# Performance work log

Hardware: AMD Instinct MI355X
Metric: run time of the kernel (lower is better)

Reference implementation:

```python
import jax, jax.numpy as jnp
import numpy as np

EPS = 1e-6
CLIP_RATIO = 1.0  # input_clip_ratio


def fwht(x):
    """Fast Walsh-Hadamard transform along last dim (N must be a power of 2).
    Unnormalized; caller divides by sqrt(N) (QuaRot OnlineHadamard convention)."""
    m, n = x.shape
    h = 1
    y = x
    while h < n:  # log2(n) fixed iterations, fine under jit
        y = y.reshape(m, n // (2 * h), 2, h)
        a, b = y[:, :, 0, :], y[:, :, 1, :]
        y = jnp.concatenate([a + b, a - b], axis=-1)  # [m, n//(2h), 2h]
        h *= 2
    return y.reshape(m, n)


def setup_inputs() -> dict:
    key = jax.random.key(0)
    k1, k2, k3 = jax.random.split(key, 3)
    M, IN, OUT = 8192, 4096, 4096
    x = jax.random.normal(k1, (M, IN), dtype=jnp.float32)
    weight = jax.random.normal(k2, (OUT, IN), dtype=jnp.float32) * 0.02
    bias = jax.random.normal(k3, (OUT,), dtype=jnp.float32) * 0.01
    return {"x": x, "weight": weight, "bias": bias}


def reference(x, weight, bias):
    # --- offline weight quantization (quantize_from_float) ---
    # per-output-row symmetric int4: scale = max|w| / 7, clamp min 1e-6
    w_scales = jnp.clip(jnp.max(jnp.abs(weight), axis=1, keepdims=True), EPS, None) / 7.0  # [OUT,1]
    qw = jnp.clip(jnp.round(weight / w_scales), -8, 7)  # int4 values kept in fp32 (exact)

    # --- online Hadamard rotation of activations ---
    n = x.shape[-1]
    x2 = fwht(x) * (1.0 / jnp.sqrt(jnp.float32(n)))

    # --- symmetric per-token int4 activation quantization (QuaRot Quantizer) ---
    sx = jnp.clip(jnp.max(jnp.abs(x2), axis=-1, keepdims=True), EPS, None) * (CLIP_RATIO / 7.0)  # [M,1]
    qx = jnp.clip(jnp.round(x2 / sx), -8, 7)

    qy = jnp.einsum('mk,nk->mn', qx, qw)  # [M, OUT]

    # --- sym_dequant: row scale (activation) * column scale (weight) + bias ---
    y = qy * sx * w_scales.T + bias[None, :]
    return y
```

## Files before the change

kernel.cpp:

```cpp
#include <hip/hip_runtime.h>
#include <hip/hip_bf16.h>
#include <cstdint>

#define QEPS 1e-6f

typedef int v4i __attribute__((ext_vector_type(4)));

__device__ __forceinline__ void gl_lds16(const void* g, void* l) {
  __builtin_amdgcn_global_load_lds(
      (const __attribute__((address_space(1))) void*)g,
      (__attribute__((address_space(3))) void*)l, 16, 0, 0);
}

__global__ __launch_bounds__(256) void wquant_kernel(const float* __restrict__ w,
                                                     int8_t* __restrict__ qw,
                                                     float* __restrict__ wscale) {
  const int n = blockIdx.x;
  const int t = threadIdx.x;
  const float4* wrow = (const float4*)(w + (size_t)n * 4096);
  float4 v[4];
  float am = 0.f;
#pragma unroll
  for (int i = 0; i < 4; ++i) {
    v[i] = wrow[i * 256 + t];
    am = fmaxf(am, fmaxf(fmaxf(fabsf(v[i].x), fabsf(v[i].y)),
                         fmaxf(fabsf(v[i].z), fabsf(v[i].w))));
  }
#pragma unroll
  for (int off = 32; off > 0; off >>= 1)
    am = fmaxf(am, __shfl_down(am, off));
  __shared__ float wm[4];
  if ((t & 63) == 0) wm[t >> 6] = am;
  __syncthreads();
  const float rowmax = fmaxf(fmaxf(wm[0], wm[1]), fmaxf(wm[2], wm[3]));
  const float scale = fmaxf(rowmax, QEPS) / 7.0f;
  if (t == 0) wscale[n] = scale;
  char4* qrow = (char4*)(qw + (size_t)n * 4096);
#pragma unroll
  for (int i = 0; i < 4; ++i) {
    char4 q;
    q.x = (signed char)fminf(fmaxf(rintf(v[i].x / scale), -8.f), 7.f);
    q.y = (signed char)fminf(fmaxf(rintf(v[i].y / scale), -8.f), 7.f);
    q.z = (signed char)fminf(fmaxf(rintf(v[i].z / scale), -8.f), 7.f);
    q.w = (signed char)fminf(fmaxf(rintf(v[i].w / scale), -8.f), 7.f);
    qrow[i * 256 + t] = q;
  }
}

__global__ __launch_bounds__(256) void xquant_kernel(const float* __restrict__ x,
                                                     int8_t* __restrict__ qx,
                                                     float* __restrict__ sx) {
  const int m = blockIdx.x;
  const int t = threadIdx.x;
  __shared__ float s[4096];
  float4* sv = (float4*)s;
  const float4* xrow = (const float4*)(x + (size_t)m * 4096);
#pragma unroll
  for (int i = 0; i < 4; ++i) sv[i * 256 + t] = xrow[i * 256 + t];
  for (int h = 1; h < 4096; h <<= 1) {
    __syncthreads();
#pragma unroll
    for (int j = 0; j < 8; ++j) {
      const int p = j * 256 + t;
      const int i0 = ((p & ~(h - 1)) << 1) | (p & (h - 1));
      const float a = s[i0];
      const float b = s[i0 + h];
      s[i0] = a + b;
      s[i0 + h] = a - b;
    }
  }
  __syncthreads();
  float4 v[4];
  float am = 0.f;
#pragma unroll
  for (int i = 0; i < 4; ++i) {
    v[i] = sv[i * 256 + t];
    am = fmaxf(am, fmaxf(fmaxf(fabsf(v[i].x), fabsf(v[i].y)),
                         fmaxf(fabsf(v[i].z), fabsf(v[i].w))));
  }
#pragma unroll
  for (int off = 32; off > 0; off >>= 1)
    am = fmaxf(am, __shfl_down(am, off));
  __shared__ float wm[4];
  if ((t & 63) == 0) wm[t >> 6] = am;
  __syncthreads();
  const float rowmax = fmaxf(fmaxf(wm[0], wm[1]), fmaxf(wm[2], wm[3]));
  const float sxv = fmaxf(rowmax * (1.0f / 64.0f), QEPS) * (float)(1.0 / 7.0);
  if (t == 0) sx[m] = sxv;
  char4* qrow = (char4*)(qx + (size_t)m * 4096);
#pragma unroll
  for (int i = 0; i < 4; ++i) {
    char4 q;
    q.x = (signed char)fminf(fmaxf(rintf((v[i].x * (1.0f / 64.0f)) / sxv), -8.f), 7.f);
    q.y = (signed char)fminf(fmaxf(rintf((v[i].y * (1.0f / 64.0f)) / sxv), -8.f), 7.f);
    q.z = (signed char)fminf(fmaxf(rintf((v[i].z * (1.0f / 64.0f)) / sxv), -8.f), 7.f);
    q.w = (signed char)fminf(fmaxf(rintf((v[i].w * (1.0f / 64.0f)) / sxv), -8.f), 7.f);
    qrow[i * 256 + t] = q;
  }
}

#define BM 128
#define BN 128
#define BK 64

__global__ __launch_bounds__(256) void gemm_kernel(const int8_t* __restrict__ qx,
                                                   const int8_t* __restrict__ qw,
                                                   const float* __restrict__ sx,
                                                   const float* __restrict__ wscale,
                                                   const float* __restrict__ bias,
                                                   float* __restrict__ out) {
  __shared__ int8_t As[BM * BK] __attribute__((aligned(16)));
  __shared__ int8_t Bs[BN * BK] __attribute__((aligned(16)));
  const int t = threadIdx.x;
  const int m0 = blockIdx.y * BM;
  const int n0 = blockIdx.x * BN;
  const int lane = t & 63;
  const int wave = t >> 6;
  const int wr = wave >> 1;
  const int wc = wave & 1;
  const int lr = lane & 15;
  const int lq = lane >> 4;

  v4i acc[4][4] = {};

  const int flat0 = t * 16;
  const int row0 = flat0 >> 6;
  const int col0 = flat0 & 63;
  const int8_t* gA0 = qx + (size_t)(m0 + row0) * 4096 + col0;
  const int8_t* gA1 = qx + (size_t)(m0 + 64 + row0) * 4096 + col0;
  const int8_t* gB0 = qw + (size_t)(n0 + row0) * 4096 + col0;
  const int8_t* gB1 = qw + (size_t)(n0 + 64 + row0) * 4096 + col0;

  for (int k0 = 0; k0 < 4096; k0 += BK) {
    __syncthreads();
    gl_lds16(gA0 + k0, As + flat0);
    gl_lds16(gA1 + k0, As + 4096 + flat0);
    gl_lds16(gB0 + k0, Bs + flat0);
    gl_lds16(gB1 + k0, Bs + 4096 + flat0);
    __syncthreads();

    v4i a[4], b[4];
#pragma unroll
    for (int mt = 0; mt < 4; ++mt)
      a[mt] = *(const v4i*)(As + (wr * 64 + mt * 16 + lr) * 64 + lq * 16);
#pragma unroll
    for (int nt = 0; nt < 4; ++nt)
      b[nt] = *(const v4i*)(Bs + (wc * 64 + nt * 16 + lr) * 64 + lq * 16);
#pragma unroll
    for (int mt = 0; mt < 4; ++mt)
#pragma unroll
      for (int nt = 0; nt < 4; ++nt)
        acc[mt][nt] = __builtin_amdgcn_mfma_i32_16x16x64_i8(a[mt], b[nt], acc[mt][nt], 0, 0, 0);
  }

#pragma unroll
  for (int mt = 0; mt < 4; ++mt) {
#pragma unroll
    for (int r = 0; r < 4; ++r) {
      const int m = m0 + wr * 64 + mt * 16 + lq * 4 + r;
      const float sm = sx[m];
#pragma unroll
      for (int nt = 0; nt < 4; ++nt) {
        const int n = n0 + wc * 64 + nt * 16 + lr;
        out[(size_t)m * 4096 + n] = (float)acc[mt][nt][r] * sm * wscale[n] + bias[n];
      }
    }
  }
}

extern "C" void kernel_launch(void* const* d_in, const int* in_sizes, int n_in,
                              void* d_out, int out_size, void* d_ws, size_t ws_size,
                              hipStream_t stream) {
  const float* x = (const float*)d_in[0];
  const float* w = (const float*)d_in[1];
  const float* bias = (const float*)d_in[2];
  float* out = (float*)d_out;

  int8_t* qx = (int8_t*)d_ws;
  int8_t* qw = qx + (size_t)8192 * 4096;
  float* wscale = (float*)(qw + (size_t)4096 * 4096);
  float* sxp = wscale + 4096;

  wquant_kernel<<<4096, 256, 0, stream>>>(w, qw, wscale);
  xquant_kernel<<<8192, 256, 0, stream>>>(x, qx, sxp);
  dim3 grid(4096 / BN, 8192 / BM);
  gemm_kernel<<<grid, 256, 0, stream>>>(qx, qw, sxp, wscale, bias, out);
}
```

Baseline: 459.7 us.

## Do per-row FWHT in registers with wave shuffles and swizzle GEMM LDS tiles

The activation Hadamard transform now runs one wavefront per row. Each lane holds 64 floats in registers and combines in-register butterflies with cross-lane xor shuffles, replacing the 12 barrier-separated shared-memory passes. This also lets the row-max reduction stay within one wave, with no shared memory. Separately, the GEMM permutes which 16-byte chunks each thread loads into LDS with an XOR swizzle and reads them back with the matching swizzle, meant to cut LDS bank conflicts on the MFMA operand reads. The register-resident transform raises VGPR pressure, and the swizzle must stay consistent between the load and read patterns.

```diff
diff --git a/kernel.cpp b/kernel.cpp
--- a/kernel.cpp
+++ b/kernel.cpp
@@ -50,52 +50,76 @@
 __global__ __launch_bounds__(256) void xquant_kernel(const float* __restrict__ x,
                                                      int8_t* __restrict__ qx,
                                                      float* __restrict__ sx) {
-  const int m = blockIdx.x;
-  const int t = threadIdx.x;
-  __shared__ float s[4096];
-  float4* sv = (float4*)s;
+  const int m = blockIdx.x * 4 + (threadIdx.x >> 6);
+  const int g = threadIdx.x & 63;
   const float4* xrow = (const float4*)(x + (size_t)m * 4096);
-#pragma unroll
-  for (int i = 0; i < 4; ++i) sv[i * 256 + t] = xrow[i * 256 + t];
-  for (int h = 1; h < 4096; h <<= 1) {
-    __syncthreads();
-#pragma unroll
-    for (int j = 0; j < 8; ++j) {
-      const int p = j * 256 + t;
-      const int i0 = ((p & ~(h - 1)) << 1) | (p & (h - 1));
-      const float a = s[i0];
-      const float b = s[i0 + h];
-      s[i0] = a + b;
-      s[i0 + h] = a - b;
+  float4 v[16];
+#pragma unroll
+  for (int j = 0; j < 16; ++j) v[j] = xrow[j * 64 + g];
+
+#pragma unroll
+  for (int j = 0; j < 16; ++j) {
+    float a0 = v[j].x, b0 = v[j].y, a1 = v[j].z, b1 = v[j].w;
+    v[j].x = a0 + b0; v[j].y = a0 - b0;
+    v[j].z = a1 + b1; v[j].w = a1 - b1;
+  }
+#pragma unroll
+  for (int j = 0; j < 16; ++j) {
+    float a0 = v[j].x, b0 = v[j].z, a1 = v[j].y, b1 = v[j].w;
+    v[j].x = a0 + b0; v[j].z = a0 - b0;
+    v[j].y = a1 + b1; v[j].w = a1 - b1;
+  }
+#pragma unroll
+  for (int d = 1; d < 64; d <<= 1) {
+    const bool low = (g & d) == 0;
+#pragma unroll
+    for (int j = 0; j < 16; ++j) {
+      float px = __shfl_xor(v[j].x, d);
+      float py = __shfl_xor(v[j].y, d);
+      float pz = __shfl_xor(v[j].z, d);
+      float pw = __shfl_xor(v[j].w, d);
+      v[j].x = low ? (v[j].x + px) : (px - v[j].x);
+      v[j].y = low ? (v[j].y + py) : (py - v[j].y);
+      v[j].z = low ? (v[j].z + pz) : (pz - v[j].z);
+      v[j].w = low ? (v[j].w + pw) : (pw - v[j].w);
     }
   }
-  __syncthreads();
-  float4 v[4];
+#pragma unroll
+  for (int d = 1; d < 16; d <<= 1) {
+#pragma unroll
+    for (int j = 0; j < 16; ++j) {
+      if ((j & d) == 0) {
+        float4 a = v[j], b = v[j + d];
+        v[j].x = a.x + b.x; v[j].y = a.y + b.y;
+        v[j].z = a.z + b.z; v[j].w = a.w + b.w;
+        v[j + d].x = a.x - b.x; v[j + d].y = a.y - b.y;
+        v[j + d].z = a.z - b.z; v[j + d].w = a.w - b.w;
+      }
+    }
+  }
+
   float am = 0.f;
 #pragma unroll
-  for (int i = 0; i < 4; ++i) {
-    v[i] = sv[i * 256 + t];
-    am = fmaxf(am, fmaxf(fmaxf(fabsf(v[i].x), fabsf(v[i].y)),
-                         fmaxf(fabsf(v[i].z), fabsf(v[i].w))));
-  }
+  for (int j = 0; j < 16; ++j)
+    am = fmaxf(am, fmaxf(fmaxf(fabsf(v[j].x), fabsf(v[j].y)),
+                         fmaxf(fabsf(v[j].z), fabsf(v[j].w))));
 #pragma unroll
   for (int off = 32; off > 0; off >>= 1)
-    am = fmaxf(am, __shfl_down(am, off));
-  __shared__ float wm[4];
-  if ((t & 63) == 0) wm[t >> 6] = am;
-  __syncthreads();
-  const float rowmax = fmaxf(fmaxf(wm[0], wm[1]), fmaxf(wm[2], wm[3]));
-  const float sxv = fmaxf(rowmax * (1.0f / 64.0f), QEPS) * (float)(1.0 / 7.0);
-  if (t == 0) sx[m] = sxv;
+    am = fmaxf(am, __shfl_xor(am, off));
+
+  const float inv64 = 1.0f / 64.0f;
+  const float sxv = fmaxf(am * inv64, QEPS) * (1.0f / 7.0f);
+  if (g == 0) sx[m] = sxv;
+
   char4* qrow = (char4*)(qx + (size_t)m * 4096);
 #pragma unroll
-  for (int i = 0; i < 4; ++i) {
+  for (int j = 0; j < 16; ++j) {
     char4 q;
-    q.x = (signed char)fminf(fmaxf(rintf((v[i].x * (1.0f / 64.0f)) / sxv), -8.f), 7.f);
-    q.y = (signed char)fminf(fmaxf(rintf((v[i].y * (1.0f / 64.0f)) / sxv), -8.f), 7.f);
-    q.z = (signed char)fminf(fmaxf(rintf((v[i].z * (1.0f / 64.0f)) / sxv), -8.f), 7.f);
-    q.w = (signed char)fminf(fmaxf(rintf((v[i].w * (1.0f / 64.0f)) / sxv), -8.f), 7.f);
-    qrow[i * 256 + t] = q;
+    q.x = (signed char)fminf(fmaxf(rintf((v[j].x * inv64) / sxv), -8.f), 7.f);
+    q.y = (signed char)fminf(fmaxf(rintf((v[j].y * inv64) / sxv), -8.f), 7.f);
+    q.z = (signed char)fminf(fmaxf(rintf((v[j].z * inv64) / sxv), -8.f), 7.f);
+    q.w = (signed char)fminf(fmaxf(rintf((v[j].w * inv64) / sxv), -8.f), 7.f);
+    qrow[j * 64 + g] = q;
   }
 }
 
@@ -125,11 +149,20 @@
 
   const int flat0 = t * 16;
   const int row0 = flat0 >> 6;
-  const int col0 = flat0 & 63;
-  const int8_t* gA0 = qx + (size_t)(m0 + row0) * 4096 + col0;
-  const int8_t* gA1 = qx + (size_t)(m0 + 64 + row0) * 4096 + col0;
-  const int8_t* gB0 = qw + (size_t)(n0 + row0) * 4096 + col0;
-  const int8_t* gB1 = qw + (size_t)(n0 + 64 + row0) * 4096 + col0;
+  const int c_src = (t & 3) ^ ((t >> 3) & 3);
+  const int goff = row0 * 4096 + c_src * 16;
+  const int8_t* gA0 = qx + (size_t)m0 * 4096 + goff;
+  const int8_t* gA1 = qx + (size_t)(m0 + 64) * 4096 + goff;
+  const int8_t* gB0 = qw + (size_t)n0 * 4096 + goff;
+  const int8_t* gB1 = qw + (size_t)(n0 + 64) * 4096 + goff;
+
+  const int swz = (lr >> 1) & 3;
+  int aoff[4], boff[4];
+#pragma unroll
+  for (int i = 0; i < 4; ++i) {
+    aoff[i] = (wr * 64 + i * 16 + lr) * 64 + ((lq ^ swz) * 16);
+    boff[i] = (wc * 64 + i * 16 + lr) * 64 + ((lq ^ swz) * 16);
+  }
 
   for (int k0 = 0; k0 < 4096; k0 += BK) {
     __syncthreads();
@@ -141,11 +174,9 @@
 
     v4i a[4], b[4];
 #pragma unroll
-    for (int mt = 0; mt < 4; ++mt)
-      a[mt] = *(const v4i*)(As + (wr * 64 + mt * 16 + lr) * 64 + lq * 16);
-#pragma unroll
-    for (int nt = 0; nt < 4; ++nt)
-      b[nt] = *(const v4i*)(Bs + (wc * 64 + nt * 16 + lr) * 64 + lq * 16);
+    for (int mt = 0; mt < 4; ++mt) a[mt] = *(const v4i*)(As + aoff[mt]);
+#pragma unroll
+    for (int nt = 0; nt < 4; ++nt) b[nt] = *(const v4i*)(Bs + boff[nt]);
 #pragma unroll
     for (int mt = 0; mt < 4; ++mt)
 #pragma unroll
@@ -182,7 +213,7 @@
   float* sxp = wscale + 4096;
 
   wquant_kernel<<<4096, 256, 0, stream>>>(w, qw, wscale);
-  xquant_kernel<<<8192, 256, 0, stream>>>(x, qx, sxp);
+  xquant_kernel<<<2048, 256, 0, stream>>>(x, qx, sxp);
   dim3 grid(4096 / BN, 8192 / BM);
   gemm_kernel<<<grid, 256, 0, stream>>>(qx, qw, sxp, wscale, bias, out);
 }
```

New measurement: 438.6 us. 4.6% less time.
